# Kernel tuning notes

Hardware: AMD Instinct MI355X
Metric: run time of the kernel (lower is better)

## Reference

```python
import jax, jax.numpy as jnp
import numpy as np

N = 50000
E = 1600000
IN_C = 128
HID = 64
HEADS = 4
OUT_C = 64
NEG_SLOPE = 0.2


def gat_layer(x, src, dst, W, a_src, a_dst, b, heads, ch):
    # x: [N, F_in], W: [F_in, heads*ch], a_src/a_dst: [heads, ch], b: [heads*ch]
    n = x.shape[0]
    h = (x @ W).reshape(n, heads, ch)                       # [N, H, C]
    alpha_s = jnp.einsum('nhc,hc->nh', h, a_src)            # [N, H]
    alpha_d = jnp.einsum('nhc,hc->nh', h, a_dst)
    e = jax.nn.leaky_relu(alpha_s[src] + alpha_d[dst], NEG_SLOPE)  # [Et, H]
    # segment softmax over incoming edges of each dst node (self-loops guarantee non-empty)
    m = jax.ops.segment_max(e, dst, num_segments=n)
    ex = jnp.exp(e - m[dst])
    denom = jax.ops.segment_sum(ex, dst, num_segments=n)
    alpha = ex / (denom[dst] + 1e-16)                       # [Et, H]
    out = jax.ops.segment_sum(h[src] * alpha[:, :, None], dst, num_segments=n)  # [N,H,C]
    return out.reshape(n, heads * ch) + b


def setup_inputs() -> dict:
    key = jax.random.key(0)
    ks = jax.random.split(key, 10)
    x = jax.random.normal(ks[0], (N, IN_C), dtype=jnp.float32)
    edge_index = jax.random.randint(ks[1], (2, E), 0, N, dtype=jnp.int64)
    s = 0.1
    W1 = jax.random.normal(ks[2], (IN_C, HEADS * HID), dtype=jnp.float32) * s
    a_src1 = jax.random.normal(ks[3], (HEADS, HID), dtype=jnp.float32) * s
    a_dst1 = jax.random.normal(ks[4], (HEADS, HID), dtype=jnp.float32) * s
    b1 = jnp.zeros((HEADS * HID,), dtype=jnp.float32)
    W2 = jax.random.normal(ks[5], (HEADS * HID, OUT_C), dtype=jnp.float32) * s
    a_src2 = jax.random.normal(ks[6], (1, OUT_C), dtype=jnp.float32) * s
    a_dst2 = jax.random.normal(ks[7], (1, OUT_C), dtype=jnp.float32) * s
    b2 = jnp.zeros((OUT_C,), dtype=jnp.float32)
    return {"x": x, "edge_index": edge_index, "W1": W1, "a_src1": a_src1,
            "a_dst1": a_dst1, "b1": b1, "W2": W2, "a_src2": a_src2,
            "a_dst2": a_dst2, "b2": b2}


def reference(x, edge_index, W1, a_src1, a_dst1, b1, W2, a_src2, a_dst2, b2):
    # add self-loops (PyG GATConv default)
    loops = jnp.arange(N, dtype=edge_index.dtype)
    src = jnp.concatenate([edge_index[0], loops])
    dst = jnp.concatenate([edge_index[1], loops])
    h = gat_layer(x, src, dst, W1, a_src1, a_dst1, b1, HEADS, HID)
    h = jax.nn.relu(h)
    out = gat_layer(h, src, dst, W2, a_src2, a_dst2, b2, 1, OUT_C)
    return out
```

## Files before the change

### kernel.cpp

```cpp
#include <hip/hip_runtime.h>
#include <cstdint>
#include <cstddef>

#define IN_C 128

typedef _Float16 __attribute__((ext_vector_type(4))) half4v;
typedef _Float16 __attribute__((ext_vector_type(8))) f16x8;
typedef float    __attribute__((ext_vector_type(4))) f32x4;

static __device__ __forceinline__ float lrelu(float x) { return x > 0.f ? x : 0.2f * x; }

static __device__ __forceinline__ float h16_to_f(unsigned short u) {
  union { unsigned short u; _Float16 h; } c; c.u = u;
  return (float)c.h;
}
static __device__ __forceinline__ unsigned pack2h(float a, float b) {
  union { _Float16 h[2]; unsigned u; } c;
  c.h[0] = (_Float16)a; c.h[1] = (_Float16)b;
  return c.u;
}

__global__ void k_zero_i32(int* __restrict__ p, int n) {
  int i = blockIdx.x * 256 + threadIdx.x;
  if (i < n) p[i] = 0;
}

__global__ void k_count(const int* __restrict__ ei_dst, int* __restrict__ cnt, int E, int Et) {
  int e = blockIdx.x * 256 + threadIdx.x;
  if (e >= Et) return;
  int d = (e < E) ? ei_dst[e] : (e - E);
  atomicAdd(&cnt[d], 1);
}

__global__ void k_scan1(const int* __restrict__ cnt, int* __restrict__ loc,
                        int* __restrict__ bsum, int n) {
  int tid = threadIdx.x;
  int i = blockIdx.x * 256 + tid;
  int v = (i < n) ? cnt[i] : 0;
  int lane = tid & 63, w = tid >> 6;
  int s = v;
#pragma unroll
  for (int off = 1; off < 64; off <<= 1) {
    int t = __shfl_up(s, off);
    if (lane >= off) s += t;
  }
  __shared__ int wt[4];
  if (lane == 63) wt[w] = s;
  __syncthreads();
  int add = 0;
#pragma unroll
  for (int k = 0; k < 4; ++k)
    if (k < w) add += wt[k];
  int incl = s + add;
  if (i < n) loc[i] = incl - v;
  if (tid == 255) bsum[blockIdx.x] = incl;
}

__global__ void k_scan2(int* __restrict__ bsum, int nb, int* __restrict__ total_out) {
  int tid = threadIdx.x;
  int v = (tid < nb) ? bsum[tid] : 0;
  int lane = tid & 63, w = tid >> 6;
  int s = v;
#pragma unroll
  for (int off = 1; off < 64; off <<= 1) {
    int t = __shfl_up(s, off);
    if (lane >= off) s += t;
  }
  __shared__ int wt[4];
  if (lane == 63) wt[w] = s;
  __syncthreads();
  int add = 0;
#pragma unroll
  for (int k = 0; k < 4; ++k)
    if (k < w) add += wt[k];
  int incl = s + add;
  if (tid < nb) bsum[tid] = incl - v;
  if (tid == 255) *total_out = incl;
}

__global__ void k_scan3(const int* __restrict__ loc, const int* __restrict__ bsum,
                        int* __restrict__ row_ptr, int* __restrict__ fill, int n) {
  int i = blockIdx.x * 256 + threadIdx.x;
  if (i < n) {
    int v = loc[i] + bsum[blockIdx.x];
    row_ptr[i] = v;
    fill[i] = v;
  }
}

__global__ void k_scatter_fused(const int* __restrict__ ei_src, const int* __restrict__ ei_dst,
                                int* __restrict__ fill,
                                const float* __restrict__ as1, const float* __restrict__ ad1,
                                uint4* __restrict__ recs, int E, int Et, int nPerReg, int n) {
  int r = blockIdx.x & 7;
  int e = (blockIdx.x >> 3) * 256 + threadIdx.x;
  if (e >= Et) return;
  int d = (e < E) ? ei_dst[e] : (e - E);
  int lo = r * nPerReg;
  int hi = (r == 7) ? n : lo + nPerReg;
  if (d < lo || d >= hi) return;
  int s = (e < E) ? ei_src[e] : d;
  int pos = atomicAdd(&fill[d], 1);
  float4 a = *(const float4*)&as1[s * 4];
  float4 b = *(const float4*)&ad1[d * 4];
  unsigned w01 = pack2h(__expf(lrelu(a.x + b.x)), __expf(lrelu(a.y + b.y)));
  unsigned w23 = pack2h(__expf(lrelu(a.z + b.z)), __expf(lrelu(a.w + b.w)));
  recs[pos] = make_uint4((unsigned)s, (unsigned)d, w01, w23);
}

__global__ void k_xh(const float* __restrict__ x, _Float16* __restrict__ xh, int n4) {
  int i = blockIdx.x * 256 + threadIdx.x;
  if (i >= n4) return;
  float4 v = *(const float4*)&x[i * 4];
  half4v o;
  o.x = (_Float16)v.x; o.y = (_Float16)v.y; o.z = (_Float16)v.z; o.w = (_Float16)v.w;
  *(half4v*)&xh[i * 4] = o;
}

__global__ void k_wt(const float* __restrict__ W, _Float16* __restrict__ Wt, int K, int N) {
  int i = blockIdx.x * 256 + threadIdx.x;
  if (i >= K * N) return;
  int k = i / N, n = i % N;
  Wt[(size_t)n * K + k] = (_Float16)W[i];
}

template <int NCG, int K>
__launch_bounds__(256)
__global__ void k_gemm_mfma(const _Float16* __restrict__ A, const _Float16* __restrict__ Bt,
                            _Float16* __restrict__ C, int M) {
  constexpr int N = NCG * 16;
  int w = threadIdx.x >> 6, lane = threadIdx.x & 63;
  int r = lane & 15, kg = lane >> 4;
  int m0 = blockIdx.x * 64 + w * 16;
  f32x4 acc[NCG];
#pragma unroll
  for (int c = 0; c < NCG; ++c) acc[c] = (f32x4){0.f, 0.f, 0.f, 0.f};
  int mA = m0 + r; if (mA > M - 1) mA = M - 1;
  const _Float16* Arow = A + (size_t)mA * K + kg * 8;
#pragma unroll
  for (int k0 = 0; k0 < K; k0 += 32) {
    f16x8 a = *(const f16x8*)(Arow + k0);
#pragma unroll
    for (int c = 0; c < NCG; ++c) {
      f16x8 b = *(const f16x8*)&Bt[(size_t)(c * 16 + r) * K + k0 + kg * 8];
      acc[c] = __builtin_amdgcn_mfma_f32_16x16x32_f16(a, b, acc[c], 0, 0, 0);
    }
  }
#pragma unroll
  for (int c = 0; c < NCG; ++c) {
#pragma unroll
    for (int j = 0; j < 4; ++j) {
      int m = m0 + kg * 4 + j;
      if (m < M) C[(size_t)m * N + c * 16 + r] = (_Float16)acc[c][j];
    }
  }
}

__launch_bounds__(256)
__global__ void k_alpha1(const _Float16* __restrict__ h1h, const float* __restrict__ a_s,
                         const float* __restrict__ a_d, float* __restrict__ as,
                         float* __restrict__ ad, int n) {
  int wave = threadIdx.x >> 6, lane = threadIdx.x & 63;
  int node = blockIdx.x * 4 + wave;
  if (node >= n) return;
  half4v hv = *(const half4v*)&h1h[(size_t)node * 256 + lane * 4];
  float4 sv = *(const float4*)&a_s[lane * 4];
  float4 dv = *(const float4*)&a_d[lane * 4];
  float h0 = (float)hv.x, h1 = (float)hv.y, h2 = (float)hv.z, h3 = (float)hv.w;
  float s = h0 * sv.x + h1 * sv.y + h2 * sv.z + h3 * sv.w;
  float d = h0 * dv.x + h1 * dv.y + h2 * dv.z + h3 * dv.w;
#pragma unroll
  for (int off = 1; off < 16; off <<= 1) { s += __shfl_xor(s, off); d += __shfl_xor(d, off); }
  if ((lane & 15) == 0) {
    as[node * 4 + (lane >> 4)] = s;
    ad[node * 4 + (lane >> 4)] = d;
  }
}

__launch_bounds__(256)
__global__ void k_alpha2(const _Float16* __restrict__ h2h, const float* __restrict__ a_s,
                         const float* __restrict__ a_d, float* __restrict__ as,
                         float* __restrict__ ad, int n) {
  int wave = threadIdx.x >> 6, lane = threadIdx.x & 63;
  int node = blockIdx.x * 4 + wave;
  if (node >= n) return;
  float hv = (float)h2h[(size_t)node * 64 + lane];
  float s = hv * a_s[lane];
  float d = hv * a_d[lane];
#pragma unroll
  for (int off = 1; off < 64; off <<= 1) { s += __shfl_xor(s, off); d += __shfl_xor(d, off); }
  if (lane == 0) { as[node] = s; ad[node] = d; }
}

__global__ void k_edgew2(const uint4* __restrict__ recs,
                         const float* __restrict__ as2, const float* __restrict__ ad2,
                         uint2* __restrict__ sw, int Et) {
  int i = blockIdx.x * 256 + threadIdx.x;
  if (i >= Et) return;
  uint4 rc = recs[i];
  int s = (int)rc.x, d = (int)rc.y;
  float z = as2[s] + ad2[d];
  uint2 o;
  o.x = rc.x;
  o.y = pack2h(__expf(lrelu(z)), 0.f) & 0xffffu;
  sw[i] = o;
}

__launch_bounds__(256)
__global__ void k_aggr1(const int* __restrict__ row_ptr, const uint4* __restrict__ recs,
                        const _Float16* __restrict__ h1h, const float* __restrict__ b1,
                        _Float16* __restrict__ hrelu_h, int n) {
  int wave = threadIdx.x >> 6, lane = threadIdx.x & 63;
  int node = blockIdx.x * 4 + wave;
  if (node >= n) return;
  int beg = row_ptr[node], end = row_ptr[node + 1];
  int g = lane >> 4, l16 = lane & 15;
  int ch0 = l16 * 16;
  int myh = l16 >> 2;
  float acc[16] = {};
  float dsum = 0.f;
  for (int i = beg; i < end; i += 4) {
    int idx = i + g;
    int s = 0; float w = 0.f;
    if (idx < end) {
      uint4 rc = recs[idx];
      s = (int)rc.x;
      unsigned wp = (myh & 2) ? rc.w : rc.z;
      w = h16_to_f((myh & 1) ? (unsigned short)(wp >> 16) : (unsigned short)(wp & 0xffffu));
    }
    const _Float16* hp = &h1h[(size_t)s * 256 + ch0];
    f16x8 hA = *(const f16x8*)hp;
    f16x8 hB = *(const f16x8*)(hp + 8);
    dsum += w;
#pragma unroll
    for (int j = 0; j < 8; ++j) acc[j] += w * (float)hA[j];
#pragma unroll
    for (int j = 0; j < 8; ++j) acc[8 + j] += w * (float)hB[j];
  }
#pragma unroll
  for (int off = 16; off < 64; off <<= 1) {
    dsum += __shfl_xor(dsum, off);
#pragma unroll
    for (int j = 0; j < 16; ++j) acc[j] += __shfl_xor(acc[j], off);
  }
  if (g == 0) {
    float inv = 1.0f / (dsum + 1e-16f);
    f16x8 oA, oB;
#pragma unroll
    for (int j = 0; j < 8; ++j) {
      oA[j] = (_Float16)fmaxf(acc[j] * inv + b1[ch0 + j], 0.f);
      oB[j] = (_Float16)fmaxf(acc[8 + j] * inv + b1[ch0 + 8 + j], 0.f);
    }
    _Float16* op = &hrelu_h[(size_t)node * 256 + ch0];
    *(f16x8*)op = oA;
    *(f16x8*)(op + 8) = oB;
  }
}

__launch_bounds__(256)
__global__ void k_aggr2(const int* __restrict__ row_ptr, const uint2* __restrict__ sw,
                        const _Float16* __restrict__ h2h, const float* __restrict__ b2,
                        float* __restrict__ out, int n) {
  int wave = threadIdx.x >> 6, lane = threadIdx.x & 63;
  int node = blockIdx.x * 4 + wave;
  if (node >= n) return;
  int beg = row_ptr[node], end = row_ptr[node + 1];
  int g = lane >> 4, l16 = lane & 15;
  int ch0 = l16 * 4;
  float acc[4] = {};
  float dsum = 0.f;
  for (int i = beg; i < end; i += 4) {
    int idx = i + g;
    int s = 0; float w = 0.f;
    if (idx < end) {
      uint2 r = sw[idx];
      s = (int)r.x;
      w = h16_to_f((unsigned short)r.y);
    }
    half4v hv = *(const half4v*)&h2h[(size_t)s * 64 + ch0];
    dsum += w;
    acc[0] += w * (float)hv.x; acc[1] += w * (float)hv.y;
    acc[2] += w * (float)hv.z; acc[3] += w * (float)hv.w;
  }
#pragma unroll
  for (int off = 16; off < 64; off <<= 1) {
    dsum += __shfl_xor(dsum, off);
#pragma unroll
    for (int j = 0; j < 4; ++j) acc[j] += __shfl_xor(acc[j], off);
  }
  if (g == 0) {
    float inv = 1.0f / (dsum + 1e-16f);
    float4 o;
    o.x = acc[0] * inv + b2[ch0];
    o.y = acc[1] * inv + b2[ch0 + 1];
    o.z = acc[2] * inv + b2[ch0 + 2];
    o.w = acc[3] * inv + b2[ch0 + 3];
    *(float4*)&out[(size_t)node * 64 + ch0] = o;
  }
}

extern "C" void kernel_launch(void* const* d_in, const int* in_sizes, int n_in,
                              void* d_out, int out_size, void* d_ws, size_t ws_size,
                              hipStream_t stream) {
  const float* x    = (const float*)d_in[0];
  const int*   ei   = (const int*)d_in[1];
  const float* W1   = (const float*)d_in[2];
  const float* a_s1 = (const float*)d_in[3];
  const float* a_d1 = (const float*)d_in[4];
  const float* b1   = (const float*)d_in[5];
  const float* W2   = (const float*)d_in[6];
  const float* a_s2 = (const float*)d_in[7];
  const float* a_d2 = (const float*)d_in[8];
  const float* b2   = (const float*)d_in[9];
  float* out = (float*)d_out;

  const int n  = in_sizes[0] / IN_C;
  const int E  = in_sizes[1] / 2;
  const int Et = E + n;
  const int* ei_src = ei;
  const int* ei_dst = ei + E;

  char* ws = (char*)d_ws;
  size_t off = 0;
  auto alloc = [&](size_t bytes) -> void* {
    void* p = ws + off;
    off = (off + bytes + 255) & ~(size_t)255;
    return p;
  };
  _Float16* xh      = (_Float16*)alloc((size_t)n * 128 * 2);
  _Float16* W1t     = (_Float16*)alloc((size_t)256 * 128 * 2);
  _Float16* W2t     = (_Float16*)alloc((size_t)64 * 256 * 2);
  _Float16* h1h     = (_Float16*)alloc((size_t)n * 256 * 2);
  _Float16* hrelu_h = (_Float16*)alloc((size_t)n * 256 * 2);
  _Float16* h2h     = (_Float16*)alloc((size_t)n * 64 * 2);
  float* as1        = (float*)alloc((size_t)n * 4 * 4);
  float* ad1        = (float*)alloc((size_t)n * 4 * 4);
  float* as2        = (float*)alloc((size_t)n * 4);
  float* ad2        = (float*)alloc((size_t)n * 4);
  int* cnt          = (int*)alloc((size_t)n * 4);
  int* loc          = (int*)alloc((size_t)n * 4);
  int* row_ptr      = (int*)alloc((size_t)(n + 1) * 4);
  int* fill         = (int*)alloc((size_t)n * 4);
  int* bsum         = (int*)alloc((size_t)256 * 4);
  uint4* recs       = (uint4*)alloc((size_t)Et * 16);
  uint2* sw2        = (uint2*)alloc((size_t)Et * 8);

  int eb  = (Et + 255) / 256;
  int nb  = (n + 255) / 256;
  int nw  = (n + 3) / 4;
  int gx1 = (n + 63) / 64;
  int nPerReg = (n + 7) / 8;

  hipLaunchKernelGGL(k_zero_i32, dim3(nb), dim3(256), 0, stream, cnt, n);
  hipLaunchKernelGGL(k_count, dim3(eb), dim3(256), 0, stream, ei_dst, cnt, E, Et);
  hipLaunchKernelGGL(k_scan1, dim3(nb), dim3(256), 0, stream, cnt, loc, bsum, n);
  hipLaunchKernelGGL(k_scan2, dim3(1), dim3(256), 0, stream, bsum, nb, row_ptr + n);
  hipLaunchKernelGGL(k_scan3, dim3(nb), dim3(256), 0, stream, loc, bsum, row_ptr, fill, n);

  hipLaunchKernelGGL(k_xh, dim3((n * 128 / 4 + 255) / 256), dim3(256), 0, stream, x, xh, n * 128 / 4);
  hipLaunchKernelGGL(k_wt, dim3((128 * 256 + 255) / 256), dim3(256), 0, stream, W1, W1t, 128, 256);
  hipLaunchKernelGGL(k_wt, dim3((256 * 64 + 255) / 256), dim3(256), 0, stream, W2, W2t, 256, 64);
  hipLaunchKernelGGL((k_gemm_mfma<16, 128>), dim3(gx1), dim3(256), 0, stream, xh, W1t, h1h, n);
  hipLaunchKernelGGL(k_alpha1, dim3(nw), dim3(256), 0, stream, h1h, a_s1, a_d1, as1, ad1, n);

  hipLaunchKernelGGL(k_scatter_fused, dim3(eb * 8), dim3(256), 0, stream,
                     ei_src, ei_dst, fill, as1, ad1, recs, E, Et, nPerReg, n);

  hipLaunchKernelGGL(k_aggr1, dim3(nw), dim3(256), 0, stream, row_ptr, recs, h1h, b1, hrelu_h, n);

  hipLaunchKernelGGL((k_gemm_mfma<4, 256>), dim3(gx1), dim3(256), 0, stream, hrelu_h, W2t, h2h, n);
  hipLaunchKernelGGL(k_alpha2, dim3(nw), dim3(256), 0, stream, h2h, a_s2, a_d2, as2, ad2, n);
  hipLaunchKernelGGL(k_edgew2, dim3(eb), dim3(256), 0, stream, recs, as2, ad2, sw2, Et);
  hipLaunchKernelGGL(k_aggr2, dim3(nw), dim3(256), 0, stream, row_ptr, sw2, h2h, b2, out, n);
}
```

Measured before the change: 417.5 us.

## Fuse attention logits into GEMMs, drop edge-weight pass, unroll aggregation loops

Computes the per-node attention logits inside the MFMA GEMM epilogues, removing the separate alpha kernels and one re-read of h. The layer-2 edge-weight kernel and its intermediate buffer are removed; aggr2 now computes exp(lrelu(as2[s]+ad2[d])) on the fly from the edge records. The scan2/scan3 pair merges into one kernel in which every block re-reduces the block sums, and the two weight transposes share one launch. Both aggregation loops take two edges per lane group per iteration to raise memory-level parallelism, at the cost of extra registers and a redundant exp per lane group in aggr2.

Result: faster. 402.3 us (-3.6%).

```diff
diff --git a/kernel.cpp b/kernel.cpp
--- a/kernel.cpp
+++ b/kernel.cpp
@@ -56,36 +56,33 @@
   if (tid == 255) bsum[blockIdx.x] = incl;
 }
 
-__global__ void k_scan2(int* __restrict__ bsum, int nb, int* __restrict__ total_out) {
-  int tid = threadIdx.x;
-  int v = (tid < nb) ? bsum[tid] : 0;
+__global__ void k_scan3b(const int* __restrict__ loc, const int* __restrict__ bsum,
+                         int* __restrict__ row_ptr, int* __restrict__ fill, int n, int nb) {
+  int tid = threadIdx.x, b = blockIdx.x;
   int lane = tid & 63, w = tid >> 6;
-  int s = v;
+  int p = 0, t = 0;
+  for (int k = tid; k < nb; k += 256) {
+    int v = bsum[k];
+    t += v;
+    if (k < b) p += v;
+  }
 #pragma unroll
   for (int off = 1; off < 64; off <<= 1) {
-    int t = __shfl_up(s, off);
-    if (lane >= off) s += t;
-  }
-  __shared__ int wt[4];
-  if (lane == 63) wt[w] = s;
+    p += __shfl_xor(p, off);
+    t += __shfl_xor(t, off);
+  }
+  __shared__ int sp_[4], st_[4];
+  if (lane == 0) { sp_[w] = p; st_[w] = t; }
   __syncthreads();
-  int add = 0;
-#pragma unroll
-  for (int k = 0; k < 4; ++k)
-    if (k < w) add += wt[k];
-  int incl = s + add;
-  if (tid < nb) bsum[tid] = incl - v;
-  if (tid == 255) *total_out = incl;
-}
-
-__global__ void k_scan3(const int* __restrict__ loc, const int* __restrict__ bsum,
-                        int* __restrict__ row_ptr, int* __restrict__ fill, int n) {
-  int i = blockIdx.x * 256 + threadIdx.x;
+  p = sp_[0] + sp_[1] + sp_[2] + sp_[3];
+  t = st_[0] + st_[1] + st_[2] + st_[3];
+  int i = b * 256 + tid;
   if (i < n) {
-    int v = loc[i] + bsum[blockIdx.x];
+    int v = loc[i] + p;
     row_ptr[i] = v;
     fill[i] = v;
   }
+  if (b == 0 && tid == 0) row_ptr[n] = t;
 }
 
 __global__ void k_scatter_fused(const int* __restrict__ ei_src, const int* __restrict__ ei_dst,
@@ -117,93 +114,145 @@
   *(half4v*)&xh[i * 4] = o;
 }
 
-__global__ void k_wt(const float* __restrict__ W, _Float16* __restrict__ Wt, int K, int N) {
+__global__ void k_wts(const float* __restrict__ W1, const float* __restrict__ W2,
+                      _Float16* __restrict__ W1t, _Float16* __restrict__ W2t) {
   int i = blockIdx.x * 256 + threadIdx.x;
-  if (i >= K * N) return;
-  int k = i / N, n = i % N;
-  Wt[(size_t)n * K + k] = (_Float16)W[i];
-}
-
-template <int NCG, int K>
+  if (i < 128 * 256) {
+    int k = i / 256, nn = i % 256;
+    W1t[(size_t)nn * 128 + k] = (_Float16)W1[i];
+  } else {
+    int j = i - 128 * 256;
+    if (j < 256 * 64) {
+      int k = j / 64, nn = j % 64;
+      W2t[(size_t)nn * 256 + k] = (_Float16)W2[j];
+    }
+  }
+}
+
 __launch_bounds__(256)
-__global__ void k_gemm_mfma(const _Float16* __restrict__ A, const _Float16* __restrict__ Bt,
-                            _Float16* __restrict__ C, int M) {
-  constexpr int N = NCG * 16;
+__global__ void k_gemm1_a(const _Float16* __restrict__ A, const _Float16* __restrict__ Bt,
+                          const float* __restrict__ a_s, const float* __restrict__ a_d,
+                          _Float16* __restrict__ C, float* __restrict__ as1,
+                          float* __restrict__ ad1, int M) {
   int w = threadIdx.x >> 6, lane = threadIdx.x & 63;
   int r = lane & 15, kg = lane >> 4;
   int m0 = blockIdx.x * 64 + w * 16;
-  f32x4 acc[NCG];
-#pragma unroll
-  for (int c = 0; c < NCG; ++c) acc[c] = (f32x4){0.f, 0.f, 0.f, 0.f};
+  f32x4 acc[16];
+#pragma unroll
+  for (int c = 0; c < 16; ++c) acc[c] = (f32x4){0.f, 0.f, 0.f, 0.f};
   int mA = m0 + r; if (mA > M - 1) mA = M - 1;
-  const _Float16* Arow = A + (size_t)mA * K + kg * 8;
-#pragma unroll
-  for (int k0 = 0; k0 < K; k0 += 32) {
+  const _Float16* Arow = A + (size_t)mA * 128 + kg * 8;
+#pragma unroll
+  for (int k0 = 0; k0 < 128; k0 += 32) {
     f16x8 a = *(const f16x8*)(Arow + k0);
 #pragma unroll
-    for (int c = 0; c < NCG; ++c) {
-      f16x8 b = *(const f16x8*)&Bt[(size_t)(c * 16 + r) * K + k0 + kg * 8];
+    for (int c = 0; c < 16; ++c) {
+      f16x8 b = *(const f16x8*)&Bt[(size_t)(c * 16 + r) * 128 + k0 + kg * 8];
       acc[c] = __builtin_amdgcn_mfma_f32_16x16x32_f16(a, b, acc[c], 0, 0, 0);
     }
   }
-#pragma unroll
-  for (int c = 0; c < NCG; ++c) {
+  float sp[4][4] = {}, dp[4][4] = {};
+#pragma unroll
+  for (int c = 0; c < 16; ++c) {
+    float asv = a_s[c * 16 + r];
+    float adv = a_d[c * 16 + r];
+#pragma unroll
+    for (int j = 0; j < 4; ++j) {
+      float v = acc[c][j];
+      sp[c >> 2][j] += v * asv;
+      dp[c >> 2][j] += v * adv;
+    }
+  }
+#pragma unroll
+  for (int off = 1; off < 16; off <<= 1) {
+#pragma unroll
+    for (int h = 0; h < 4; ++h)
+#pragma unroll
+      for (int j = 0; j < 4; ++j) {
+        sp[h][j] += __shfl_xor(sp[h][j], off);
+        dp[h][j] += __shfl_xor(dp[h][j], off);
+      }
+  }
+#pragma unroll
+  for (int c = 0; c < 16; ++c) {
 #pragma unroll
     for (int j = 0; j < 4; ++j) {
       int m = m0 + kg * 4 + j;
-      if (m < M) C[(size_t)m * N + c * 16 + r] = (_Float16)acc[c][j];
+      if (m < M) C[(size_t)m * 256 + c * 16 + r] = (_Float16)acc[c][j];
+    }
+  }
+  if (r == 0) {
+#pragma unroll
+    for (int j = 0; j < 4; ++j) {
+      int m = m0 + kg * 4 + j;
+      if (m < M) {
+#pragma unroll
+        for (int h = 0; h < 4; ++h) {
+          as1[m * 4 + h] = sp[h][j];
+          ad1[m * 4 + h] = dp[h][j];
+        }
+      }
     }
   }
 }
 
 __launch_bounds__(256)
-__global__ void k_alpha1(const _Float16* __restrict__ h1h, const float* __restrict__ a_s,
-                         const float* __restrict__ a_d, float* __restrict__ as,
-                         float* __restrict__ ad, int n) {
-  int wave = threadIdx.x >> 6, lane = threadIdx.x & 63;
-  int node = blockIdx.x * 4 + wave;
-  if (node >= n) return;
-  half4v hv = *(const half4v*)&h1h[(size_t)node * 256 + lane * 4];
-  float4 sv = *(const float4*)&a_s[lane * 4];
-  float4 dv = *(const float4*)&a_d[lane * 4];
-  float h0 = (float)hv.x, h1 = (float)hv.y, h2 = (float)hv.z, h3 = (float)hv.w;
-  float s = h0 * sv.x + h1 * sv.y + h2 * sv.z + h3 * sv.w;
-  float d = h0 * dv.x + h1 * dv.y + h2 * dv.z + h3 * dv.w;
-#pragma unroll
-  for (int off = 1; off < 16; off <<= 1) { s += __shfl_xor(s, off); d += __shfl_xor(d, off); }
-  if ((lane & 15) == 0) {
-    as[node * 4 + (lane >> 4)] = s;
-    ad[node * 4 + (lane >> 4)] = d;
-  }
-}
-
-__launch_bounds__(256)
-__global__ void k_alpha2(const _Float16* __restrict__ h2h, const float* __restrict__ a_s,
-                         const float* __restrict__ a_d, float* __restrict__ as,
-                         float* __restrict__ ad, int n) {
-  int wave = threadIdx.x >> 6, lane = threadIdx.x & 63;
-  int node = blockIdx.x * 4 + wave;
-  if (node >= n) return;
-  float hv = (float)h2h[(size_t)node * 64 + lane];
-  float s = hv * a_s[lane];
-  float d = hv * a_d[lane];
-#pragma unroll
-  for (int off = 1; off < 64; off <<= 1) { s += __shfl_xor(s, off); d += __shfl_xor(d, off); }
-  if (lane == 0) { as[node] = s; ad[node] = d; }
-}
-
-__global__ void k_edgew2(const uint4* __restrict__ recs,
-                         const float* __restrict__ as2, const float* __restrict__ ad2,
-                         uint2* __restrict__ sw, int Et) {
-  int i = blockIdx.x * 256 + threadIdx.x;
-  if (i >= Et) return;
-  uint4 rc = recs[i];
-  int s = (int)rc.x, d = (int)rc.y;
-  float z = as2[s] + ad2[d];
-  uint2 o;
-  o.x = rc.x;
-  o.y = pack2h(__expf(lrelu(z)), 0.f) & 0xffffu;
-  sw[i] = o;
+__global__ void k_gemm2_a(const _Float16* __restrict__ A, const _Float16* __restrict__ Bt,
+                          const float* __restrict__ a_s, const float* __restrict__ a_d,
+                          _Float16* __restrict__ C, float* __restrict__ as2,
+                          float* __restrict__ ad2, int M) {
+  int w = threadIdx.x >> 6, lane = threadIdx.x & 63;
+  int r = lane & 15, kg = lane >> 4;
+  int m0 = blockIdx.x * 64 + w * 16;
+  f32x4 acc[4];
+#pragma unroll
+  for (int c = 0; c < 4; ++c) acc[c] = (f32x4){0.f, 0.f, 0.f, 0.f};
+  int mA = m0 + r; if (mA > M - 1) mA = M - 1;
+  const _Float16* Arow = A + (size_t)mA * 256 + kg * 8;
+#pragma unroll
+  for (int k0 = 0; k0 < 256; k0 += 32) {
+    f16x8 a = *(const f16x8*)(Arow + k0);
+#pragma unroll
+    for (int c = 0; c < 4; ++c) {
+      f16x8 b = *(const f16x8*)&Bt[(size_t)(c * 16 + r) * 256 + k0 + kg * 8];
+      acc[c] = __builtin_amdgcn_mfma_f32_16x16x32_f16(a, b, acc[c], 0, 0, 0);
+    }
+  }
+  float sp[4] = {}, dp[4] = {};
+#pragma unroll
+  for (int c = 0; c < 4; ++c) {
+    float asv = a_s[c * 16 + r];
+    float adv = a_d[c * 16 + r];
+#pragma unroll
+    for (int j = 0; j < 4; ++j) {
+      float v = acc[c][j];
+      sp[j] += v * asv;
+      dp[j] += v * adv;
+    }
+  }
+#pragma unroll
+  for (int off = 1; off < 16; off <<= 1) {
+#pragma unroll
+    for (int j = 0; j < 4; ++j) {
+      sp[j] += __shfl_xor(sp[j], off);
+      dp[j] += __shfl_xor(dp[j], off);
+    }
+  }
+#pragma unroll
+  for (int c = 0; c < 4; ++c) {
+#pragma unroll
+    for (int j = 0; j < 4; ++j) {
+      int m = m0 + kg * 4 + j;
+      if (m < M) C[(size_t)m * 64 + c * 16 + r] = (_Float16)acc[c][j];
+    }
+  }
+  if (r == 0) {
+#pragma unroll
+    for (int j = 0; j < 4; ++j) {
+      int m = m0 + kg * 4 + j;
+      if (m < M) { as2[m] = sp[j]; ad2[m] = dp[j]; }
+    }
+  }
 }
 
 __launch_bounds__(256)
@@ -219,23 +268,37 @@
   int myh = l16 >> 2;
   float acc[16] = {};
   float dsum = 0.f;
-  for (int i = beg; i < end; i += 4) {
-    int idx = i + g;
-    int s = 0; float w = 0.f;
-    if (idx < end) {
-      uint4 rc = recs[idx];
-      s = (int)rc.x;
+  for (int i = beg; i < end; i += 8) {
+    int iA = i + g, iB = i + 4 + g;
+    int sA = 0, sB = 0;
+    float wA = 0.f, wB = 0.f;
+    if (iA < end) {
+      uint4 rc = recs[iA];
+      sA = (int)rc.x;
       unsigned wp = (myh & 2) ? rc.w : rc.z;
-      w = h16_to_f((myh & 1) ? (unsigned short)(wp >> 16) : (unsigned short)(wp & 0xffffu));
-    }
-    const _Float16* hp = &h1h[(size_t)s * 256 + ch0];
-    f16x8 hA = *(const f16x8*)hp;
-    f16x8 hB = *(const f16x8*)(hp + 8);
-    dsum += w;
-#pragma unroll
-    for (int j = 0; j < 8; ++j) acc[j] += w * (float)hA[j];
-#pragma unroll
-    for (int j = 0; j < 8; ++j) acc[8 + j] += w * (float)hB[j];
+      wA = h16_to_f((myh & 1) ? (unsigned short)(wp >> 16) : (unsigned short)(wp & 0xffffu));
+    }
+    if (iB < end) {
+      uint4 rc = recs[iB];
+      sB = (int)rc.x;
+      unsigned wp = (myh & 2) ? rc.w : rc.z;
+      wB = h16_to_f((myh & 1) ? (unsigned short)(wp >> 16) : (unsigned short)(wp & 0xffffu));
+    }
+    const _Float16* pA = &h1h[(size_t)sA * 256 + ch0];
+    const _Float16* pB = &h1h[(size_t)sB * 256 + ch0];
+    f16x8 a0 = *(const f16x8*)pA;
+    f16x8 a1 = *(const f16x8*)(pA + 8);
+    f16x8 c0 = *(const f16x8*)pB;
+    f16x8 c1 = *(const f16x8*)(pB + 8);
+    dsum += wA + wB;
+#pragma unroll
+    for (int j = 0; j < 8; ++j) acc[j] += wA * (float)a0[j];
+#pragma unroll
+    for (int j = 0; j < 8; ++j) acc[8 + j] += wA * (float)a1[j];
+#pragma unroll
+    for (int j = 0; j < 8; ++j) acc[j] += wB * (float)c0[j];
+#pragma unroll
+    for (int j = 0; j < 8; ++j) acc[8 + j] += wB * (float)c1[j];
   }
 #pragma unroll
   for (int off = 16; off < 64; off <<= 1) {
@@ -258,29 +321,38 @@
 }
 
 __launch_bounds__(256)
-__global__ void k_aggr2(const int* __restrict__ row_ptr, const uint2* __restrict__ sw,
+__global__ void k_aggr2(const int* __restrict__ row_ptr, const uint4* __restrict__ recs,
+                        const float* __restrict__ as2, const float* __restrict__ ad2,
                         const _Float16* __restrict__ h2h, const float* __restrict__ b2,
                         float* __restrict__ out, int n) {
   int wave = threadIdx.x >> 6, lane = threadIdx.x & 63;
   int node = blockIdx.x * 4 + wave;
   if (node >= n) return;
   int beg = row_ptr[node], end = row_ptr[node + 1];
+  float adm = ad2[node];
   int g = lane >> 4, l16 = lane & 15;
   int ch0 = l16 * 4;
   float acc[4] = {};
   float dsum = 0.f;
-  for (int i = beg; i < end; i += 4) {
-    int idx = i + g;
-    int s = 0; float w = 0.f;
-    if (idx < end) {
-      uint2 r = sw[idx];
-      s = (int)r.x;
-      w = h16_to_f((unsigned short)r.y);
-    }
-    half4v hv = *(const half4v*)&h2h[(size_t)s * 64 + ch0];
-    dsum += w;
-    acc[0] += w * (float)hv.x; acc[1] += w * (float)hv.y;
-    acc[2] += w * (float)hv.z; acc[3] += w * (float)hv.w;
+  for (int i = beg; i < end; i += 8) {
+    int iA = i + g, iB = i + 4 + g;
+    int sA = 0, sB = 0;
+    float wA = 0.f, wB = 0.f;
+    if (iA < end) {
+      sA = (int)recs[iA].x;
+      wA = __expf(lrelu(as2[sA] + adm));
+    }
+    if (iB < end) {
+      sB = (int)recs[iB].x;
+      wB = __expf(lrelu(as2[sB] + adm));
+    }
+    half4v hA = *(const half4v*)&h2h[(size_t)sA * 64 + ch0];
+    half4v hB = *(const half4v*)&h2h[(size_t)sB * 64 + ch0];
+    dsum += wA + wB;
+    acc[0] += wA * (float)hA.x + wB * (float)hB.x;
+    acc[1] += wA * (float)hA.y + wB * (float)hB.y;
+    acc[2] += wA * (float)hA.z + wB * (float)hB.z;
+    acc[3] += wA * (float)hA.w + wB * (float)hB.w;
   }
 #pragma unroll
   for (int off = 16; off < 64; off <<= 1) {
@@ -343,7 +415,6 @@
   int* fill         = (int*)alloc((size_t)n * 4);
   int* bsum         = (int*)alloc((size_t)256 * 4);
   uint4* recs       = (uint4*)alloc((size_t)Et * 16);
-  uint2* sw2        = (uint2*)alloc((size_t)Et * 8);
 
   int eb  = (Et + 255) / 256;
   int nb  = (n + 255) / 256;
@@ -354,22 +425,20 @@
   hipLaunchKernelGGL(k_zero_i32, dim3(nb), dim3(256), 0, stream, cnt, n);
   hipLaunchKernelGGL(k_count, dim3(eb), dim3(256), 0, stream, ei_dst, cnt, E, Et);
   hipLaunchKernelGGL(k_scan1, dim3(nb), dim3(256), 0, stream, cnt, loc, bsum, n);
-  hipLaunchKernelGGL(k_scan2, dim3(1), dim3(256), 0, stream, bsum, nb, row_ptr + n);
-  hipLaunchKernelGGL(k_scan3, dim3(nb), dim3(256), 0, stream, loc, bsum, row_ptr, fill, n);
+  hipLaunchKernelGGL(k_scan3b, dim3(nb), dim3(256), 0, stream, loc, bsum, row_ptr, fill, n, nb);
 
   hipLaunchKernelGGL(k_xh, dim3((n * 128 / 4 + 255) / 256), dim3(256), 0, stream, x, xh, n * 128 / 4);
-  hipLaunchKernelGGL(k_wt, dim3((128 * 256 + 255) / 256), dim3(256), 0, stream, W1, W1t, 128, 256);
-  hipLaunchKernelGGL(k_wt, dim3((256 * 64 + 255) / 256), dim3(256), 0, stream, W2, W2t, 256, 64);
-  hipLaunchKernelGGL((k_gemm_mfma<16, 128>), dim3(gx1), dim3(256), 0, stream, xh, W1t, h1h, n);
-  hipLaunchKernelGGL(k_alpha1, dim3(nw), dim3(256), 0, stream, h1h, a_s1, a_d1, as1, ad1, n);
-
+  hipLaunchKernelGGL(k_wts, dim3((128 * 256 + 256 * 64 + 255) / 256), dim3(256), 0, stream,
+                     W1, W2, W1t, W2t);
+
+  hipLaunchKernelGGL(k_gemm1_a, dim3(gx1), dim3(256), 0, stream,
+                     xh, W1t, a_s1, a_d1, h1h, as1, ad1, n);
   hipLaunchKernelGGL(k_scatter_fused, dim3(eb * 8), dim3(256), 0, stream,
                      ei_src, ei_dst, fill, as1, ad1, recs, E, Et, nPerReg, n);
-
   hipLaunchKernelGGL(k_aggr1, dim3(nw), dim3(256), 0, stream, row_ptr, recs, h1h, b1, hrelu_h, n);
 
-  hipLaunchKernelGGL((k_gemm_mfma<4, 256>), dim3(gx1), dim3(256), 0, stream, hrelu_h, W2t, h2h, n);
-  hipLaunchKernelGGL(k_alpha2, dim3(nw), dim3(256), 0, stream, h2h, a_s2, a_d2, as2, ad2, n);
-  hipLaunchKernelGGL(k_edgew2, dim3(eb), dim3(256), 0, stream, recs, as2, ad2, sw2, Et);
-  hipLaunchKernelGGL(k_aggr2, dim3(nw), dim3(256), 0, stream, row_ptr, sw2, h2h, b2, out, n);
-}
+  hipLaunchKernelGGL(k_gemm2_a, dim3(gx1), dim3(256), 0, stream,
+                     hrelu_h, W2t, a_s2, a_d2, h2h, as2, ad2, n);
+  hipLaunchKernelGGL(k_aggr2, dim3(nw), dim3(256), 0, stream,
+                     row_ptr, recs, as2, ad2, h2h, b2, out, n);
+}
```
